# Kernel tuning notes

Hardware: AMD Instinct MI355X
Metric: run time of the kernel (lower is better)

Reference implementation:

```python
import jax, jax.numpy as jnp
import numpy as np

N_NODES = 50000
N_EDGES = 800000
HEADS = 6
LEAKY = 0.2


def gat_layer(x, W, a_src, a_dst, src, dst):
    """Multi-head GAT layer (Velickovic et al.), concat heads + ELU.
    x: [N, F_in], W: [H, F_in, F_out], a_src/a_dst: [H, F_out]."""
    n = x.shape[0]
    h = jnp.einsum('nf,hfo->nho', x, W)              # [N, H, F_out]
    es = jnp.einsum('nho,ho->nh', h, a_src)          # source attention term
    ed = jnp.einsum('nho,ho->nh', h, a_dst)          # destination attention term
    e = jax.nn.leaky_relu(es[src] + ed[dst], LEAKY)  # [E, H] per-edge logits
    # segment softmax over incoming edges of each destination node
    emax = jax.ops.segment_max(e, dst, num_segments=n)
    emax = jnp.where(jnp.isfinite(emax), emax, jnp.zeros_like(emax))
    ex = jnp.exp(e - emax[dst])                      # [E, H]
    denom = jax.ops.segment_sum(ex, dst, num_segments=n)
    alpha = ex / (denom[dst] + 1e-16)                # [E, H]
    msg = alpha[:, :, None] * h[src]                 # [E, H, F_out]
    out = jax.ops.segment_sum(msg, dst, num_segments=n)  # [N, H, F_out]
    return jax.nn.elu(out).reshape(n, -1)            # concat heads


def setup_inputs() -> dict:
    key = jax.random.key(0)
    ks = jax.random.split(key, 16)
    glorot = lambda k, shape: jax.random.normal(k, shape, jnp.float32) * np.sqrt(2.0 / (shape[-2] + shape[-1]))
    inp = {
        'x': jax.random.normal(ks[0], (N_NODES, 11), jnp.float32),
        'edge_index': jax.random.randint(ks[1], (2, N_EDGES), 0, N_NODES, jnp.int32),
        'W1': glorot(ks[2], (HEADS, 11, 16)),
        'a1s': glorot(ks[3], (HEADS, 16)),
        'a1d': glorot(ks[4], (HEADS, 16)),
        'W2': glorot(ks[5], (HEADS, 96, 32)),
        'a2s': glorot(ks[6], (HEADS, 32)),
        'a2d': glorot(ks[7], (HEADS, 32)),
        'W3': glorot(ks[8], (HEADS, 192, 64)),
        'a3s': glorot(ks[9], (HEADS, 64)),
        'a3d': glorot(ks[10], (HEADS, 64)),
        'Wd': glorot(ks[11], (384, 1)),
        'bd': jnp.zeros((1,), jnp.float32),
    }
    return inp


def reference(x, edge_index, W1, a1s, a1d, W2, a2s, a2d, W3, a3s, a3d, Wd, bd):
    src, dst = edge_index[0], edge_index[1]
    h = gat_layer(x, W1, a1s, a1d, src, dst)   # [N, 96]
    h = gat_layer(h, W2, a2s, a2d, src, dst)   # [N, 192]
    h = gat_layer(h, W3, a3s, a3d, src, dst)   # [N, 384]
    g = jnp.sum(h, axis=0).reshape(1, -1)      # sum pool -> [1, 384]
    g = g / jnp.maximum(jnp.linalg.norm(g, axis=1, keepdims=True), 1e-12)  # F.normalize
    out = g @ Wd + bd                          # Dense 384->1, linear nonlin
    return jnp.squeeze(out, 1)                 # [1]
```

## Files before the change

kernel.cpp:

```cpp
#include <hip/hip_runtime.h>
#include <hip/hip_bf16.h>


#define HHEADS 6

typedef __attribute__((ext_vector_type(8))) short bf16x8;
typedef __attribute__((ext_vector_type(4))) float f32x4;
typedef __attribute__((ext_vector_type(2))) float f32x2;

typedef __attribute__((address_space(3))) unsigned int lds_uint;
typedef const __attribute__((address_space(1))) unsigned int glb_uint;

__device__ __forceinline__ float bfl(unsigned u) { return __uint_as_float(u << 16); }
__device__ __forceinline__ float bfh(unsigned u) { return __uint_as_float(u & 0xffff0000u); }
__device__ __forceinline__ unsigned short f2bf(float v) {
    unsigned u = __float_as_uint(v);
    return (unsigned short)((u + 0x7fffu + ((u >> 16) & 1u)) >> 16);
}
__device__ __forceinline__ float bf2f(unsigned short h) {
    return __uint_as_float((unsigned)h << 16);
}
__device__ __forceinline__ unsigned fkey(float f) {
    unsigned u = __float_as_uint(f);
    return (u >> 31) ? ~u : (u | 0x80000000u);
}
__device__ __forceinline__ float funkey(unsigned k) {
    return (k >> 31) ? __uint_as_float(k & 0x7fffffffu) : __uint_as_float(~k);
}

__device__ __forceinline__ void xpose4(float& v0, float& v1, float& v2, float& v3, int b) {
    bool hi = (b & 2) != 0;
    float s0 = hi ? v0 : v2;
    float s1 = hi ? v1 : v3;
    s0 = __shfl_xor(s0, 2, 64);
    s1 = __shfl_xor(s1, 2, 64);
    v0 = hi ? s0 : v0;
    v1 = hi ? s1 : v1;
    v2 = hi ? v2 : s0;
    v3 = hi ? v3 : s1;
    bool od = (b & 1) != 0;
    float t0 = od ? v0 : v1;
    t0 = __shfl_xor(t0, 1, 64);
    v0 = od ? t0 : v0;
    v1 = od ? v1 : t0;
    float t1 = od ? v2 : v3;
    t1 = __shfl_xor(t1, 1, 64);
    v2 = od ? t1 : v2;
    v3 = od ? v3 : t1;
}

__global__ void zero_misc(int* __restrict__ count, int* __restrict__ cursor,
                          float* __restrict__ gmid, unsigned* __restrict__ gmax,
                          unsigned short* __restrict__ apH,
                          long pad3_off, long pad3_cnt, long pad6_off, long pad6_cnt, int n) {
    long i = (long)blockIdx.x * blockDim.x + threadIdx.x;
    long stride = (long)gridDim.x * blockDim.x;
    for (long j = i; j < n; j += stride) {
        count[j] = 0;
        cursor[j] = 0;
    }
    for (long j = i; j < 64 * 384; j += stride) gmid[j] = 0.f;
    if (i < 12) gmax[i] = 0u;
    for (long j = i; j < pad3_cnt; j += stride) apH[pad3_off + j] = 0;
    for (long j = i; j < pad6_cnt; j += stride) apH[pad6_off + j] = 0;
}

__global__ void hist_kernel(const int* __restrict__ dst, int* __restrict__ count, int E) {
    int e = blockIdx.x * blockDim.x + threadIdx.x;
    if (e >= E) return;
    atomicAdd(&count[dst[e]], 1);
}

__global__ void scan_block(const int* __restrict__ count, int* __restrict__ offsets,
                           int* __restrict__ bsum, int n) {
    __shared__ int s[1024];
    int i = blockIdx.x * 1024 + threadIdx.x;
    int v = (i < n) ? count[i] : 0;
    s[threadIdx.x] = v;
    __syncthreads();
    for (int off = 1; off < 1024; off <<= 1) {
        int t = (threadIdx.x >= (unsigned)off) ? s[threadIdx.x - off] : 0;
        __syncthreads();
        s[threadIdx.x] += t;
        __syncthreads();
    }
    if (i < n) offsets[i] = s[threadIdx.x] - v;
    if (threadIdx.x == 1023) bsum[blockIdx.x] = s[1023];
}

__global__ void scan_tops(int* __restrict__ bsum, int nb) {
    __shared__ int s[64];
    int t = threadIdx.x;
    int v = (t < nb) ? bsum[t] : 0;
    s[t] = v;
    __syncthreads();
    for (int off = 1; off < 64; off <<= 1) {
        int tmp = (t >= off) ? s[t - off] : 0;
        __syncthreads();
        s[t] += tmp;
        __syncthreads();
    }
    if (t < nb) bsum[t] = s[t] - v;
}

__global__ void scan_add(int* __restrict__ offsets, const int* __restrict__ bsum, int n,
                         int total) {
    int i = blockIdx.x * 1024 + threadIdx.x;
    if (i < n) offsets[i] += bsum[blockIdx.x];
    if (i == 0) offsets[n] = total;
}

__global__ void scatter_kernel(const int* __restrict__ src, const int* __restrict__ dst,
                               const int* __restrict__ offsets, int* __restrict__ cursor,
                               int* __restrict__ ssrc, int E) {
    int e = blockIdx.x * blockDim.x + threadIdx.x;
    if (e >= E) return;
    int d = dst[e];
    int pos = offsets[d] + atomicAdd(&cursor[d], 1);
    ssrc[pos] = src[e];
}

__global__ void repack_w(const float* __restrict__ W, float* __restrict__ Wp, int FIN, int F) {
    int HF = HHEADS * F;
    int i = blockIdx.x * blockDim.x + threadIdx.x;
    if (i >= FIN * HF) return;
    int k = i / HF, c = i % HF;
    int hd = c / F, f = c % F;
    Wp[i] = W[(hd * FIN + k) * F + f];
}

__global__ void repack_w_mfma(const float* __restrict__ W, unsigned short* __restrict__ bh,
                              int FIN, int F, int NPAD) {
    int i = blockIdx.x * blockDim.x + threadIdx.x;
    if (i >= FIN * NPAD) return;
    int k = i / NPAD, n = i % NPAD;
    int NKT = FIN / 32;
    int HF = HHEADS * F;
    float w = 0.f;
    if (n < HF) {
        int hd = n / F, f = n % F;
        w = W[(hd * FIN + k) * F + f];
    }
    size_t e = ((size_t)((n >> 4) * NKT + (k >> 5)) * 64 + ((n & 15) | (((k >> 3) & 3) << 4))) * 8 +
               (k & 7);
    bh[e] = f2bf(w);
}

template <int BM, int BN, int BK>
__global__ __launch_bounds__(256) void gemm_small_attn(const float* __restrict__ A,
                                                       const float* __restrict__ B,
                                                       unsigned char* __restrict__ C8,
                                                       const float* __restrict__ as_,
                                                       const float* __restrict__ ad_,
                                                       float* __restrict__ es,
                                                       float* __restrict__ ed, int M, int K,
                                                       int N) {
    __shared__ float As[BK][BM + 4];
    __shared__ float Bs[BK][BN];
    int tid = threadIdx.x;
    int tx = tid % 16, ty = tid / 16;
    int m0 = blockIdx.y * BM, n0 = blockIdx.x * BN;
    float acc[4][4] = {};
    for (int kk0 = 0; kk0 < K; kk0 += BK) {
#pragma unroll
        for (int i = 0; i < (BM * BK) / 256; ++i) {
            int idx = tid + i * 256;
            int m = idx / BK, k = idx % BK;
            float v = 0.f;
            if (m0 + m < M && kk0 + k < K) v = A[(size_t)(m0 + m) * K + kk0 + k];
            As[k][m] = v;
        }
#pragma unroll
        for (int i = 0; i < (BK * BN) / 1024; ++i) {
            int idx = tid + i * 256;
            int k = idx / (BN / 4), n4 = idx % (BN / 4);
            float4 v = make_float4(0.f, 0.f, 0.f, 0.f);
            if (kk0 + k < K && n0 + n4 * 4 < N)
                v = *(const float4*)&B[(size_t)(kk0 + k) * N + n0 + n4 * 4];
            *(float4*)&Bs[k][n4 * 4] = v;
        }
        __syncthreads();
#pragma unroll
        for (int k = 0; k < BK; ++k) {
            float4 av = *(const float4*)&As[k][ty * 4];
            float4 bv = *(const float4*)&Bs[k][tx * 4];
            float a[4] = {av.x, av.y, av.z, av.w};
            float b[4] = {bv.x, bv.y, bv.z, bv.w};
#pragma unroll
            for (int i = 0; i < 4; ++i)
#pragma unroll
                for (int j = 0; j < 4; ++j) acc[i][j] += a[i] * b[j];
        }
        __syncthreads();
    }
    bool colok = (n0 + tx * 4) < N;
    float asv[4], adv[4];
#pragma unroll
    for (int j = 0; j < 4; ++j) {
        int col = n0 + tx * 4 + j;
        asv[j] = (col < N) ? as_[col] : 0.f;
        adv[j] = (col < N) ? ad_[col] : 0.f;
    }
#pragma unroll
    for (int i = 0; i < 4; ++i) {
        int m = m0 + ty * 4 + i;
        bool mok = m < M;
        if (mok && colok) {
            int pk = __builtin_amdgcn_cvt_pk_fp8_f32(acc[i][0], acc[i][1], 0, false);
            pk = __builtin_amdgcn_cvt_pk_fp8_f32(acc[i][2], acc[i][3], pk, true);
            *(unsigned*)&C8[(size_t)m * N + n0 + tx * 4] = (unsigned)pk;
        }
        float ps = 0.f, pd = 0.f;
#pragma unroll
        for (int j = 0; j < 4; ++j) {
            ps += acc[i][j] * asv[j];
            pd += acc[i][j] * adv[j];
        }
        ps += __shfl_down(ps, 2, 4);
        ps += __shfl_down(ps, 1, 4);
        pd += __shfl_down(pd, 2, 4);
        pd += __shfl_down(pd, 1, 4);
        if (mok && colok && (tx & 3) == 0) {
            int hd = (n0 + tx * 4) >> 4;
            es[(size_t)m * HHEADS + hd] = ps;
            ed[(size_t)m * HHEADS + hd] = pd;
        }
    }
}

template <int K, int NREAL, int NPAD, int F, int MT>
__global__ __launch_bounds__(256) void gemm_attn_mfma(
    const unsigned short* __restrict__ Ah, const unsigned short* __restrict__ Bh,
    unsigned char* __restrict__ C8, const float* __restrict__ as_,
    const float* __restrict__ ad_, float* __restrict__ es, float* __restrict__ ed,
    unsigned* __restrict__ gmax, int M) {
    constexpr int NKT = K / 32;
    __shared__ unsigned short sB[NKT * 4096];
    __shared__ unsigned short sA[2][4096];
    int tid = threadIdx.x;
    int lane = tid & 63, wave = tid >> 6;
    int wrow = wave >> 1, wcol = wave & 1;
    int quad = lane >> 4, c16 = lane & 15;

    int nwg = gridDim.x * gridDim.y;
    int hh = blockIdx.y * gridDim.x + blockIdx.x;
    int q = nwg >> 3, r = nwg & 7;
    int xcd = hh & 7, pos = hh >> 3;
    int wk = (xcd < r ? xcd * (q + 1) : r * (q + 1) + (xcd - r) * q) + pos;
    int bx = wk % gridDim.x, by = wk / gridDim.x;

    int n0 = bx * 128;
    int bn16 = n0 >> 4;
    int nmt = (M + 127) >> 7;

#pragma unroll
    for (int kt2 = 0; kt2 < NKT; ++kt2) {
#pragma unroll
        for (int rep = 0; rep < 2; ++rep) {
            int chunk = tid + rep * 256;
            int tile = chunk >> 6, e8 = chunk & 63;
            size_t boff = ((size_t)((bn16 + tile) * NKT + kt2) * 64 + e8) * 8;
            __builtin_amdgcn_global_load_lds((glb_uint*)&Bh[boff],
                                             (lds_uint*)&sB[kt2 * 4096 + chunk * 8], 16, 0, 0);
        }
    }
    auto STAGE_A = [&](int mti, int kt2, int buf) {
#pragma unroll
        for (int rep = 0; rep < 2; ++rep) {
            int chunk = tid + rep * 256;
            int tile = chunk >> 6, e8 = chunk & 63;
            size_t aoff = ((size_t)((mti * 8 + tile) * NKT + kt2) * 64 + e8) * 8;
            __builtin_amdgcn_global_load_lds((glb_uint*)&Ah[aoff],
                                             (lds_uint*)&sA[buf][chunk * 8], 16, 0, 0);
        }
    };
    STAGE_A(min(by * MT, nmt - 1), 0, 0);
    asm volatile("s_waitcnt vmcnt(0)" ::: "memory");
    __builtin_amdgcn_s_barrier();

    float asv[4], adv[4];
#pragma unroll
    for (int j = 0; j < 4; ++j) {
        int col = n0 + wcol * 64 + j * 16 + c16;
        bool ok = col < NREAL;
        asv[j] = ok ? as_[col] : 0.f;
        adv[j] = ok ? ad_[col] : 0.f;
    }
    float mx = -1e30f;
    float mxA = -1e30f, mxB = -1e30f;
    bool colvalid = (n0 + wcol * 64) < NREAL;
    int b4 = lane & 3;

    f32x4 acc[4][4] = {};
    const int T = MT * NKT;
    int mt = 0, kt = 0;
    for (int t = 0; t < T; ++t) {
        int cur = t & 1;
        int nkt = kt + 1, nmt2 = mt;
        if (nkt == NKT) {
            nkt = 0;
            nmt2 = mt + 1;
        }
        if (t + 1 < T) STAGE_A(min(by * MT + nmt2, nmt - 1), nkt, cur ^ 1);
        bf16x8 fah[4], fbh[4];
#pragma unroll
        for (int i = 0; i < 4; ++i) {
            fah[i] = *(const bf16x8*)&sA[cur][(wrow * 4 + i) * 512 + lane * 8];
            fbh[i] = *(const bf16x8*)&sB[kt * 4096 + (wcol * 4 + i) * 512 + lane * 8];
        }
        asm volatile("s_waitcnt lgkmcnt(0)" ::: "memory");
        __builtin_amdgcn_sched_barrier(0);
#pragma unroll
        for (int i = 0; i < 4; ++i)
#pragma unroll
            for (int j = 0; j < 4; ++j)
                acc[i][j] = __builtin_amdgcn_mfma_f32_16x16x32_bf16(fah[i], fbh[j], acc[i][j],
                                                                    0, 0, 0);
        if (kt == NKT - 1) {
            int m0 = (by * MT + mt) * 128;
            if (m0 < M) {
#pragma unroll
                for (int i = 0; i < 4; ++i) {
#pragma unroll
                    for (int r2 = 0; r2 < 4; ++r2) {
                        int m = m0 + wrow * 64 + i * 16 + quad * 4 + r2;
                        bool mok = m < M;
                        if (F == 64) {
                            float ps = acc[i][0][r2] * asv[0] + acc[i][1][r2] * asv[1] +
                                       acc[i][2][r2] * asv[2] + acc[i][3][r2] * asv[3];
                            float pd = acc[i][0][r2] * adv[0] + acc[i][1][r2] * adv[1] +
                                       acc[i][2][r2] * adv[2] + acc[i][3][r2] * adv[3];
#pragma unroll
                            for (int off = 8; off > 0; off >>= 1) {
                                ps += __shfl_down(ps, off, 16);
                                pd += __shfl_down(pd, off, 16);
                            }
                            if (mok && c16 == 0) {
                                int hd = (n0 + wcol * 64) / 64;
                                es[(size_t)m * HHEADS + hd] = ps;
                                ed[(size_t)m * HHEADS + hd] = pd;
                                mx = fmaxf(mx, ps);
                            }
                        } else {
                            float psA = acc[i][0][r2] * asv[0] + acc[i][1][r2] * asv[1];
                            float pdA = acc[i][0][r2] * adv[0] + acc[i][1][r2] * adv[1];
                            float psB = acc[i][2][r2] * asv[2] + acc[i][3][r2] * asv[3];
                            float pdB = acc[i][2][r2] * adv[2] + acc[i][3][r2] * adv[3];
#pragma unroll
                            for (int off = 8; off > 0; off >>= 1) {
                                psA += __shfl_down(psA, off, 16);
                                pdA += __shfl_down(pdA, off, 16);
                                psB += __shfl_down(psB, off, 16);
                                pdB += __shfl_down(pdB, off, 16);
                            }
                            if (mok && c16 == 0 && colvalid) {
                                int colbase = n0 + wcol * 64;
                                int hd = colbase / 32;
                                es[(size_t)m * HHEADS + hd] = psA;
                                ed[(size_t)m * HHEADS + hd] = pdA;
                                es[(size_t)m * HHEADS + hd + 1] = psB;
                                ed[(size_t)m * HHEADS + hd + 1] = pdB;
                                mxA = fmaxf(mxA, psA);
                                mxB = fmaxf(mxB, psB);
                            }
                        }
                    }
                }
#pragma unroll
                for (int i = 0; i < 4; ++i) {
                    int m = m0 + wrow * 64 + i * 16 + quad * 4 + b4;
                    bool mok = m < M;
#pragma unroll
                    for (int j = 0; j < 4; ++j) {
                        float v0 = acc[i][j][0], v1 = acc[i][j][1], v2 = acc[i][j][2],
                              v3 = acc[i][j][3];
                        xpose4(v0, v1, v2, v3, b4);
                        int colb = n0 + wcol * 64 + j * 16 + (c16 & 12);
                        if (mok && (F == 64 || colvalid)) {
                            int pk = __builtin_amdgcn_cvt_pk_fp8_f32(v0, v1, 0, false);
                            pk = __builtin_amdgcn_cvt_pk_fp8_f32(v2, v3, pk, true);
                            *(unsigned*)&C8[(size_t)m * NREAL + colb] = (unsigned)pk;
                        }
                    }
                }
            }
#pragma unroll
            for (int i = 0; i < 4; ++i)
#pragma unroll
                for (int j = 0; j < 4; ++j) acc[i][j] = (f32x4){0.f, 0.f, 0.f, 0.f};
        }
        asm volatile("s_waitcnt vmcnt(0)" ::: "memory");
        __builtin_amdgcn_s_barrier();
        kt = nkt;
        mt = nmt2;
    }

    if (F == 64) {
#pragma unroll
        for (int off = 32; off > 0; off >>= 1) mx = fmaxf(mx, __shfl_xor(mx, off));
        if (lane == 0) atomicMax(&gmax[(n0 + wcol * 64) / 64], fkey(mx));
    } else {
        mxA = fmaxf(mxA, __shfl_xor(mxA, 16));
        mxA = fmaxf(mxA, __shfl_xor(mxA, 32));
        mxB = fmaxf(mxB, __shfl_xor(mxB, 16));
        mxB = fmaxf(mxB, __shfl_xor(mxB, 32));
        if (lane == 0 && colvalid) {
            int hd = (n0 + wcol * 64) / 32;
            atomicMax(&gmax[6 + hd], fkey(mxA));
            atomicMax(&gmax[6 + hd + 1], fkey(mxB));
        }
    }
}

template <int F>
__global__ __launch_bounds__(256) void aggregate_fused(
    const unsigned char* __restrict__ h8, const float* __restrict__ es,
    const float* __restrict__ ed, const int* __restrict__ offsets,
    const int* __restrict__ ssrc, unsigned short* __restrict__ oh, int n) {
    constexpr int HF = HHEADS * F;
    constexpr int C8 = HF / 8;
    int tid = blockIdx.x * blockDim.x + threadIdx.x;
    if (tid >= n * C8) return;
    int node = tid / C8, q = tid % C8;
    int c = q * 8, hd = c / F;
    int a = offsets[node], b = offsets[node + 1];
    float edv = ed[node * HHEADS + hd];
    float m = -1e30f, l = 0.f;
    f32x2 a0 = {0.f, 0.f}, a1 = {0.f, 0.f}, a2 = {0.f, 0.f}, a3 = {0.f, 0.f};
    for (int j = a; j < b; ++j) {
        int s = ssrc[j];
        float v = es[s * HHEADS + hd] + edv;
        v = v > 0.f ? v : 0.2f * v;
        float mn = fmaxf(m, v);
        float r = __expf(m - mn);
        float wgt = __expf(v - mn);
        uint2 hv = *(const uint2*)&h8[(size_t)s * HF + c];
        f32x2 p0 = __builtin_amdgcn_cvt_pk_f32_fp8((int)hv.x, false);
        f32x2 p1 = __builtin_amdgcn_cvt_pk_f32_fp8((int)hv.x, true);
        f32x2 p2 = __builtin_amdgcn_cvt_pk_f32_fp8((int)hv.y, false);
        f32x2 p3 = __builtin_amdgcn_cvt_pk_f32_fp8((int)hv.y, true);
        l = l * r + wgt;
        f32x2 rv = {r, r}, wv = {wgt, wgt};
        a0 = a0 * rv + wv * p0;
        a1 = a1 * rv + wv * p1;
        a2 = a2 * rv + wv * p2;
        a3 = a3 * rv + wv * p3;
        m = mn;
    }
    float invd = 1.0f / (l + 1e-16f);
    float res[8] = {a0[0], a0[1], a1[0], a1[1], a2[0], a2[1], a3[0], a3[1]};
    unsigned short th[8];
#pragma unroll
    for (int k = 0; k < 8; ++k) {
        float v = res[k] * invd;
        v = v > 0.f ? v : (__expf(v) - 1.0f);
        th[k] = f2bf(v);
    }
    constexpr int NKT = HF / 32;
    int lq = (node & 15) | (((c >> 3) & 3) << 4);
    size_t base = ((size_t)((node >> 4) * NKT + (c >> 5)) * 64 + lq) * 8;
    *(uint4*)&oh[base] = *(uint4*)th;
}

__global__ __launch_bounds__(256) void aggregate_wpn2(
    const unsigned char* __restrict__ h8, const float* __restrict__ es,
    const float* __restrict__ ed, const unsigned* __restrict__ gmax,
    const int* __restrict__ offsets, const int* __restrict__ ssrc,
    unsigned short* __restrict__ oh, int n) {
    constexpr int HF = 192;
    int wid = (int)((blockIdx.x * (unsigned)blockDim.x + threadIdx.x) >> 6);
    int lane = threadIdx.x & 63;
    if (wid >= n || lane >= 48) return;
    int node = wid;
    int hd = lane >> 3;
    int c = lane * 4;
    int a = offsets[node], b = offsets[node + 1];
    float edv = ed[node * HHEADS + hd];
    float mv = funkey(gmax[6 + hd]) + edv;
    float m = mv > 0.f ? mv : 0.2f * mv;
    float l = 0.f;
    f32x2 a0 = {0.f, 0.f}, a1 = {0.f, 0.f};
    const unsigned char* hbase = h8 + c;
    int j = a;
    for (; j + 3 < b; j += 4) {
        int s0 = ssrc[j], s1 = ssrc[j + 1], s2 = ssrc[j + 2], s3 = ssrc[j + 3];
        float ev0 = es[(size_t)s0 * HHEADS + hd];
        float ev1 = es[(size_t)s1 * HHEADS + hd];
        float ev2 = es[(size_t)s2 * HHEADS + hd];
        float ev3 = es[(size_t)s3 * HHEADS + hd];
        unsigned h0 = *(const unsigned*)(hbase + (size_t)s0 * HF);
        unsigned h1 = *(const unsigned*)(hbase + (size_t)s1 * HF);
        unsigned h2 = *(const unsigned*)(hbase + (size_t)s2 * HF);
        unsigned h3 = *(const unsigned*)(hbase + (size_t)s3 * HF);
        float v0 = ev0 + edv;
        v0 = v0 > 0.f ? v0 : 0.2f * v0;
        float v1 = ev1 + edv;
        v1 = v1 > 0.f ? v1 : 0.2f * v1;
        float v2 = ev2 + edv;
        v2 = v2 > 0.f ? v2 : 0.2f * v2;
        float v3 = ev3 + edv;
        v3 = v3 > 0.f ? v3 : 0.2f * v3;
        float w0 = __expf(v0 - m);
        float w1 = __expf(v1 - m);
        float w2 = __expf(v2 - m);
        float w3 = __expf(v3 - m);
        {
            f32x2 p0 = __builtin_amdgcn_cvt_pk_f32_fp8((int)h0, false);
            f32x2 p1 = __builtin_amdgcn_cvt_pk_f32_fp8((int)h0, true);
            f32x2 wv = {w0, w0};
            l += w0;
            a0 = a0 + wv * p0;
            a1 = a1 + wv * p1;
        }
        {
            f32x2 p0 = __builtin_amdgcn_cvt_pk_f32_fp8((int)h1, false);
            f32x2 p1 = __builtin_amdgcn_cvt_pk_f32_fp8((int)h1, true);
            f32x2 wv = {w1, w1};
            l += w1;
            a0 = a0 + wv * p0;
            a1 = a1 + wv * p1;
        }
        {
            f32x2 p0 = __builtin_amdgcn_cvt_pk_f32_fp8((int)h2, false);
            f32x2 p1 = __builtin_amdgcn_cvt_pk_f32_fp8((int)h2, true);
            f32x2 wv = {w2, w2};
            l += w2;
            a0 = a0 + wv * p0;
            a1 = a1 + wv * p1;
        }
        {
            f32x2 p0 = __builtin_amdgcn_cvt_pk_f32_fp8((int)h3, false);
            f32x2 p1 = __builtin_amdgcn_cvt_pk_f32_fp8((int)h3, true);
            f32x2 wv = {w3, w3};
            l += w3;
            a0 = a0 + wv * p0;
            a1 = a1 + wv * p1;
        }
    }
    for (; j < b; ++j) {
        int s0 = ssrc[j];
        float ev0 = es[(size_t)s0 * HHEADS + hd];
        unsigned h0 = *(const unsigned*)(hbase + (size_t)s0 * HF);
        float v0 = ev0 + edv;
        v0 = v0 > 0.f ? v0 : 0.2f * v0;
        float w0 = __expf(v0 - m);
        f32x2 p0 = __builtin_amdgcn_cvt_pk_f32_fp8((int)h0, false);
        f32x2 p1 = __builtin_amdgcn_cvt_pk_f32_fp8((int)h0, true);
        f32x2 wv = {w0, w0};
        l += w0;
        a0 = a0 + wv * p0;
        a1 = a1 + wv * p1;
    }
    float invd = 1.0f / (l + 1e-16f);
    float res[4] = {a0[0], a0[1], a1[0], a1[1]};
    unsigned short th[4];
#pragma unroll
    for (int k = 0; k < 4; ++k) {
        float v = res[k] * invd;
        v = v > 0.f ? v : (__expf(v) - 1.0f);
        th[k] = f2bf(v);
    }
    int lq = (node & 15) | (((c >> 3) & 3) << 4);
    size_t base = ((size_t)((node >> 4) * (HF / 32) + (c >> 5)) * 64 + lq) * 8 + (c & 7);
    *(uint2*)&oh[base] = *(uint2*)th;
}

__global__ __launch_bounds__(256) void aggregate_wpn3(
    const unsigned char* __restrict__ h8, const float* __restrict__ es,
    const float* __restrict__ ed, const unsigned* __restrict__ gmax,
    const int* __restrict__ offsets, const int* __restrict__ ssrc,
    float* __restrict__ gmid, int n) {
    constexpr int HF = 384;
    __shared__ float gp[4][384];
    int wave = threadIdx.x >> 6, lane = threadIdx.x & 63;
    int wid = blockIdx.x * 4 + wave;
    int node = wid;
    int hd = lane >> 3;
    int c = lane * 8;
    bool active = (wid < n) && (lane < 48);
    float res[8] = {};
    if (active) {
        int a = offsets[node], b = offsets[node + 1];
        float edv = ed[node * HHEADS + hd];
        float mv = funkey(gmax[hd]) + edv;
        float m = mv > 0.f ? mv : 0.2f * mv;
        float l = 0.f;
        f32x2 a0 = {0.f, 0.f}, a1 = {0.f, 0.f}, a2 = {0.f, 0.f}, a3 = {0.f, 0.f};
        const unsigned char* hbase = h8 + c;
        int j = a;
        for (; j + 3 < b; j += 4) {
            int s0 = ssrc[j], s1 = ssrc[j + 1], s2 = ssrc[j + 2], s3 = ssrc[j + 3];
            float ev0 = es[(size_t)s0 * HHEADS + hd];
            float ev1 = es[(size_t)s1 * HHEADS + hd];
            float ev2 = es[(size_t)s2 * HHEADS + hd];
            float ev3 = es[(size_t)s3 * HHEADS + hd];
            uint2 h0 = *(const uint2*)(hbase + (size_t)s0 * HF);
            uint2 h1 = *(const uint2*)(hbase + (size_t)s1 * HF);
            uint2 h2 = *(const uint2*)(hbase + (size_t)s2 * HF);
            uint2 h3 = *(const uint2*)(hbase + (size_t)s3 * HF);
            float v0 = ev0 + edv;
            v0 = v0 > 0.f ? v0 : 0.2f * v0;
            float v1 = ev1 + edv;
            v1 = v1 > 0.f ? v1 : 0.2f * v1;
            float v2 = ev2 + edv;
            v2 = v2 > 0.f ? v2 : 0.2f * v2;
            float v3 = ev3 + edv;
            v3 = v3 > 0.f ? v3 : 0.2f * v3;
            float w0 = __expf(v0 - m);
            float w1 = __expf(v1 - m);
            float w2 = __expf(v2 - m);
            float w3 = __expf(v3 - m);
            {
                f32x2 p0 = __builtin_amdgcn_cvt_pk_f32_fp8((int)h0.x, false);
                f32x2 p1 = __builtin_amdgcn_cvt_pk_f32_fp8((int)h0.x, true);
                f32x2 p2 = __builtin_amdgcn_cvt_pk_f32_fp8((int)h0.y, false);
                f32x2 p3 = __builtin_amdgcn_cvt_pk_f32_fp8((int)h0.y, true);
                f32x2 wv = {w0, w0};
                l += w0;
                a0 = a0 + wv * p0;
                a1 = a1 + wv * p1;
                a2 = a2 + wv * p2;
                a3 = a3 + wv * p3;
            }
            {
                f32x2 p0 = __builtin_amdgcn_cvt_pk_f32_fp8((int)h1.x, false);
                f32x2 p1 = __builtin_amdgcn_cvt_pk_f32_fp8((int)h1.x, true);
                f32x2 p2 = __builtin_amdgcn_cvt_pk_f32_fp8((int)h1.y, false);
                f32x2 p3 = __builtin_amdgcn_cvt_pk_f32_fp8((int)h1.y, true);
                f32x2 wv = {w1, w1};
                l += w1;
                a0 = a0 + wv * p0;
                a1 = a1 + wv * p1;
                a2 = a2 + wv * p2;
                a3 = a3 + wv * p3;
            }
            {
                f32x2 p0 = __builtin_amdgcn_cvt_pk_f32_fp8((int)h2.x, false);
                f32x2 p1 = __builtin_amdgcn_cvt_pk_f32_fp8((int)h2.x, true);
                f32x2 p2 = __builtin_amdgcn_cvt_pk_f32_fp8((int)h2.y, false);
                f32x2 p3 = __builtin_amdgcn_cvt_pk_f32_fp8((int)h2.y, true);
                f32x2 wv = {w2, w2};
                l += w2;
                a0 = a0 + wv * p0;
                a1 = a1 + wv * p1;
                a2 = a2 + wv * p2;
                a3 = a3 + wv * p3;
            }
            {
                f32x2 p0 = __builtin_amdgcn_cvt_pk_f32_fp8((int)h3.x, false);
                f32x2 p1 = __builtin_amdgcn_cvt_pk_f32_fp8((int)h3.x, true);
                f32x2 p2 = __builtin_amdgcn_cvt_pk_f32_fp8((int)h3.y, false);
                f32x2 p3 = __builtin_amdgcn_cvt_pk_f32_fp8((int)h3.y, true);
                f32x2 wv = {w3, w3};
                l += w3;
                a0 = a0 + wv * p0;
                a1 = a1 + wv * p1;
                a2 = a2 + wv * p2;
                a3 = a3 + wv * p3;
            }
        }
        for (; j < b; ++j) {
            int s0 = ssrc[j];
            float ev0 = es[(size_t)s0 * HHEADS + hd];
            uint2 h0 = *(const uint2*)(hbase + (size_t)s0 * HF);
            float v0 = ev0 + edv;
            v0 = v0 > 0.f ? v0 : 0.2f * v0;
            float w0 = __expf(v0 - m);
            f32x2 p0 = __builtin_amdgcn_cvt_pk_f32_fp8((int)h0.x, false);
            f32x2 p1 = __builtin_amdgcn_cvt_pk_f32_fp8((int)h0.x, true);
            f32x2 p2 = __builtin_amdgcn_cvt_pk_f32_fp8((int)h0.y, false);
            f32x2 p3 = __builtin_amdgcn_cvt_pk_f32_fp8((int)h0.y, true);
            f32x2 wv = {w0, w0};
            l += w0;
            a0 = a0 + wv * p0;
            a1 = a1 + wv * p1;
            a2 = a2 + wv * p2;
            a3 = a3 + wv * p3;
        }
        float invd = 1.0f / (l + 1e-16f);
        float t[8] = {a0[0], a0[1], a1[0], a1[1], a2[0], a2[1], a3[0], a3[1]};
#pragma unroll
        for (int k = 0; k < 8; ++k) {
            float v = t[k] * invd;
            res[k] = v > 0.f ? v : (__expf(v) - 1.0f);
        }
    }
    if (lane < 48) {
#pragma unroll
        for (int k = 0; k < 8; ++k) gp[wave][c + k] = res[k];
    }
    __syncthreads();
    int rep = blockIdx.x & 63;
    for (int i = threadIdx.x; i < 384; i += 256) {
        float s = gp[0][i] + gp[1][i] + gp[2][i] + gp[3][i];
        atomicAdd(&gmid[rep * 384 + i], s);
    }
}

__global__ void final_kernel(const float* __restrict__ gmid, const float* __restrict__ Wd,
                             const float* __restrict__ bd, float* __restrict__ outp) {
    __shared__ float red[384];
    int t = threadIdx.x;
    float v = 0.f;
    for (int r = 0; r < 64; ++r) v += gmid[r * 384 + t];
    red[t] = v * v;
    __syncthreads();
    for (int s = 192; s >= 3; s >>= 1) {
        if (t < s) red[t] += red[t + s];
        __syncthreads();
    }
    __shared__ float scale_s;
    if (t == 0) {
        float norm = sqrtf(red[0] + red[1] + red[2]);
        scale_s = 1.0f / fmaxf(norm, 1e-12f);
    }
    __syncthreads();
    float scale = scale_s;
    red[t] = v * scale * Wd[t];
    __syncthreads();
    for (int s = 192; s >= 3; s >>= 1) {
        if (t < s) red[t] += red[t + s];
        __syncthreads();
    }
    if (t == 0) outp[0] = red[0] + red[1] + red[2] + bd[0];
}

extern "C" void kernel_launch(void* const* d_in, const int* in_sizes, int n_in, void* d_out,
                              int out_size, void* d_ws, size_t ws_size, hipStream_t stream) {
    const float* x = (const float*)d_in[0];
    const int* ei = (const int*)d_in[1];
    const float* W1 = (const float*)d_in[2];
    const float* a1s = (const float*)d_in[3];
    const float* a1d = (const float*)d_in[4];
    const float* W2 = (const float*)d_in[5];
    const float* a2s = (const float*)d_in[6];
    const float* a2d = (const float*)d_in[7];
    const float* W3 = (const float*)d_in[8];
    const float* a3s = (const float*)d_in[9];
    const float* a3d = (const float*)d_in[10];
    const float* Wd = (const float*)d_in[11];
    const float* bd = (const float*)d_in[12];
    float* outp = (float*)d_out;

    const int N = in_sizes[0] / 11;
    const int E = in_sizes[1] / 2;
    const int* src = ei;
    const int* dst = ei + E;

    const int NT16 = ((N + 127) / 128) * 8;
    const int NMT = (N + 127) / 128;

    char* w = (char*)d_ws;
    size_t off = 0;
    auto A = [&](size_t bytes) {
        size_t o = off;
        off += (bytes + 255) & ~(size_t)255;
        return o;
    };
    unsigned char* bufH = (unsigned char*)(w + A((size_t)N * 384 * 2));
    float* gmid = (float*)(w + A((size_t)N * 384 * 2));
    unsigned short* apH = (unsigned short*)(w + A((size_t)NT16 * 6 * 512 * 2));
    unsigned short* b2H = (unsigned short*)(w + A((size_t)16 * 3 * 512 * 2));
    unsigned short* b3H = (unsigned short*)(w + A((size_t)24 * 6 * 512 * 2));
    float* es = (float*)(w + A((size_t)N * HHEADS * 4));
    float* ed = (float*)(w + A((size_t)N * HHEADS * 4));
    unsigned* gmax = (unsigned*)(w + A(256));
    float* wp = (float*)(w + A((size_t)11 * 96 * 4));
    int* count = (int*)(w + A((size_t)(N + 1) * 4));
    int* cursor = (int*)(w + A((size_t)(N + 1) * 4));
    int* offsets = (int*)(w + A((size_t)(N + 1) * 4));
    int* bsum = (int*)(w + A(64 * 4));
    int* ssrc = (int*)(w + A((size_t)E * 4));

    const long t16v = N / 16;
    const long padT = NT16 - t16v;
    zero_misc<<<(N + 255) / 256, 256, 0, stream>>>(count, cursor, gmid, gmax, apH,
                                                   t16v * 3 * 512, padT * 3 * 512,
                                                   t16v * 6 * 512, padT * 6 * 512, N);

    hist_kernel<<<(E + 255) / 256, 256, 0, stream>>>(dst, count, E);
    int nb = (N + 1023) / 1024;
    scan_block<<<nb, 1024, 0, stream>>>(count, offsets, bsum, N);
    scan_tops<<<1, 64, 0, stream>>>(bsum, nb);
    scan_add<<<nb, 1024, 0, stream>>>(offsets, bsum, N, E);
    scatter_kernel<<<(E + 255) / 256, 256, 0, stream>>>(src, dst, offsets, cursor, ssrc, E);

    repack_w<<<(11 * 96 + 255) / 256, 256, 0, stream>>>(W1, wp, 11, 16);
    repack_w_mfma<<<(96 * 256 + 255) / 256, 256, 0, stream>>>(W2, b2H, 96, 32, 256);
    repack_w_mfma<<<(192 * 384 + 255) / 256, 256, 0, stream>>>(W3, b3H, 192, 64, 384);

    {
        dim3 grid((96 + 63) / 64, (N + 63) / 64);
        gemm_small_attn<64, 64, 32><<<grid, 256, 0, stream>>>(x, wp, bufH, a1s, a1d, es, ed, N,
                                                              11, 96);
    }
    {
        long total = (long)N * (96 / 8);
        aggregate_fused<16><<<(total + 255) / 256, 256, 0, stream>>>(bufH, es, ed, offsets,
                                                                     ssrc, apH, N);
    }

    {
        dim3 grid(2, (NMT + 3) / 4);
        gemm_attn_mfma<96, 192, 256, 32, 4><<<grid, 256, 0, stream>>>(apH, b2H, bufH, a2s,
                                                                      a2d, es, ed, gmax, N);
    }
    {
        int grid = (N + 3) / 4;
        aggregate_wpn2<<<grid, 256, 0, stream>>>(bufH, es, ed, gmax, offsets, ssrc, apH, N);
    }

    {
        dim3 grid(3, (NMT + 3) / 4);
        gemm_attn_mfma<192, 384, 384, 64, 4><<<grid, 256, 0, stream>>>(apH, b3H, bufH, a3s,
                                                                       a3d, es, ed, gmax, N);
    }
    {
        int grid = (N + 3) / 4;
        aggregate_wpn3<<<grid, 256, 0, stream>>>(bufH, es, ed, gmax, offsets, ssrc, gmid, N);
    }

    final_kernel<<<1, 384, 0, stream>>>(gmid, Wd, bd, outp);
}
```

Baseline: 432.5 us.

## Replace LDS-staged MFMA GEMM with per-wave direct-from-global tiles

The layer-2 and layer-3 feature GEMMs no longer stage A and B through LDS with double buffering and barriers. Each wave now computes an independent 64x64 output tile, loading its MFMA fragments straight from global memory, and the attention-score and fp8 epilogue is kept but runs per wave. This removes LDS traffic, barriers and the serial multi-tile loop, and launches many more small workgroups for parallelism. In exchange, B tiles are re-read from global or L2 by every wave, there is no prefetch overlap, and there are more atomicMax operations on gmax.

```diff
diff --git a/kernel.cpp b/kernel.cpp
--- a/kernel.cpp
+++ b/kernel.cpp
@@ -7,9 +7,6 @@
 typedef __attribute__((ext_vector_type(8))) short bf16x8;
 typedef __attribute__((ext_vector_type(4))) float f32x4;
 typedef __attribute__((ext_vector_type(2))) float f32x2;
-
-typedef __attribute__((address_space(3))) unsigned int lds_uint;
-typedef const __attribute__((address_space(1))) unsigned int glb_uint;
 
 __device__ __forceinline__ float bfl(unsigned u) { return __uint_as_float(u << 16); }
 __device__ __forceinline__ float bfh(unsigned u) { return __uint_as_float(u & 0xffff0000u); }
@@ -228,186 +225,124 @@
     }
 }
 
-template <int K, int NREAL, int NPAD, int F, int MT>
-__global__ __launch_bounds__(256) void gemm_attn_mfma(
+template <int K, int NREAL, int F>
+__global__ __launch_bounds__(256) void gemm_attn_dw(
     const unsigned short* __restrict__ Ah, const unsigned short* __restrict__ Bh,
     unsigned char* __restrict__ C8, const float* __restrict__ as_,
     const float* __restrict__ ad_, float* __restrict__ es, float* __restrict__ ed,
-    unsigned* __restrict__ gmax, int M) {
+    unsigned* __restrict__ gmax, int M, int nwaves, int nstrips) {
     constexpr int NKT = K / 32;
-    __shared__ unsigned short sB[NKT * 4096];
-    __shared__ unsigned short sA[2][4096];
-    int tid = threadIdx.x;
-    int lane = tid & 63, wave = tid >> 6;
-    int wrow = wave >> 1, wcol = wave & 1;
-    int quad = lane >> 4, c16 = lane & 15;
-
-    int nwg = gridDim.x * gridDim.y;
-    int hh = blockIdx.y * gridDim.x + blockIdx.x;
-    int q = nwg >> 3, r = nwg & 7;
-    int xcd = hh & 7, pos = hh >> 3;
-    int wk = (xcd < r ? xcd * (q + 1) : r * (q + 1) + (xcd - r) * q) + pos;
-    int bx = wk % gridDim.x, by = wk / gridDim.x;
-
-    int n0 = bx * 128;
-    int bn16 = n0 >> 4;
-    int nmt = (M + 127) >> 7;
-
-#pragma unroll
-    for (int kt2 = 0; kt2 < NKT; ++kt2) {
-#pragma unroll
-        for (int rep = 0; rep < 2; ++rep) {
-            int chunk = tid + rep * 256;
-            int tile = chunk >> 6, e8 = chunk & 63;
-            size_t boff = ((size_t)((bn16 + tile) * NKT + kt2) * 64 + e8) * 8;
-            __builtin_amdgcn_global_load_lds((glb_uint*)&Bh[boff],
-                                             (lds_uint*)&sB[kt2 * 4096 + chunk * 8], 16, 0, 0);
-        }
-    }
-    auto STAGE_A = [&](int mti, int kt2, int buf) {
-#pragma unroll
-        for (int rep = 0; rep < 2; ++rep) {
-            int chunk = tid + rep * 256;
-            int tile = chunk >> 6, e8 = chunk & 63;
-            size_t aoff = ((size_t)((mti * 8 + tile) * NKT + kt2) * 64 + e8) * 8;
-            __builtin_amdgcn_global_load_lds((glb_uint*)&Ah[aoff],
-                                             (lds_uint*)&sA[buf][chunk * 8], 16, 0, 0);
-        }
-    };
-    STAGE_A(min(by * MT, nmt - 1), 0, 0);
-    asm volatile("s_waitcnt vmcnt(0)" ::: "memory");
-    __builtin_amdgcn_s_barrier();
+    int gw = blockIdx.x * 4 + (threadIdx.x >> 6);
+    if (gw >= nwaves) return;
+    int lane = threadIdx.x & 63;
+    int quad = lane >> 4, c16 = lane & 15, b4 = lane & 3;
+    int strip = gw / nstrips, cs = gw - strip * nstrips;
+    int n0 = cs * 64;
+    int at16 = strip * 4, bt16 = cs * 4;
+
+    f32x4 acc[4][4] = {};
+#pragma unroll
+    for (int kt = 0; kt < NKT; ++kt) {
+        bf16x8 fah[4], fbh[4];
+#pragma unroll
+        for (int i = 0; i < 4; ++i)
+            fah[i] = *(const bf16x8*)&Ah[((size_t)(at16 + i) * NKT + kt) * 512 + lane * 8];
+#pragma unroll
+        for (int j = 0; j < 4; ++j)
+            fbh[j] = *(const bf16x8*)&Bh[((size_t)(bt16 + j) * NKT + kt) * 512 + lane * 8];
+#pragma unroll
+        for (int i = 0; i < 4; ++i)
+#pragma unroll
+            for (int j = 0; j < 4; ++j)
+                acc[i][j] = __builtin_amdgcn_mfma_f32_16x16x32_bf16(fah[i], fbh[j], acc[i][j],
+                                                                    0, 0, 0);
+    }
 
     float asv[4], adv[4];
 #pragma unroll
     for (int j = 0; j < 4; ++j) {
-        int col = n0 + wcol * 64 + j * 16 + c16;
+        int col = n0 + j * 16 + c16;
         bool ok = col < NREAL;
         asv[j] = ok ? as_[col] : 0.f;
         adv[j] = ok ? ad_[col] : 0.f;
     }
     float mx = -1e30f;
     float mxA = -1e30f, mxB = -1e30f;
-    bool colvalid = (n0 + wcol * 64) < NREAL;
-    int b4 = lane & 3;
-
-    f32x4 acc[4][4] = {};
-    const int T = MT * NKT;
-    int mt = 0, kt = 0;
-    for (int t = 0; t < T; ++t) {
-        int cur = t & 1;
-        int nkt = kt + 1, nmt2 = mt;
-        if (nkt == NKT) {
-            nkt = 0;
-            nmt2 = mt + 1;
-        }
-        if (t + 1 < T) STAGE_A(min(by * MT + nmt2, nmt - 1), nkt, cur ^ 1);
-        bf16x8 fah[4], fbh[4];
-#pragma unroll
-        for (int i = 0; i < 4; ++i) {
-            fah[i] = *(const bf16x8*)&sA[cur][(wrow * 4 + i) * 512 + lane * 8];
-            fbh[i] = *(const bf16x8*)&sB[kt * 4096 + (wcol * 4 + i) * 512 + lane * 8];
-        }
-        asm volatile("s_waitcnt lgkmcnt(0)" ::: "memory");
-        __builtin_amdgcn_sched_barrier(0);
-#pragma unroll
-        for (int i = 0; i < 4; ++i)
-#pragma unroll
-            for (int j = 0; j < 4; ++j)
-                acc[i][j] = __builtin_amdgcn_mfma_f32_16x16x32_bf16(fah[i], fbh[j], acc[i][j],
-                                                                    0, 0, 0);
-        if (kt == NKT - 1) {
-            int m0 = (by * MT + mt) * 128;
-            if (m0 < M) {
-#pragma unroll
-                for (int i = 0; i < 4; ++i) {
-#pragma unroll
-                    for (int r2 = 0; r2 < 4; ++r2) {
-                        int m = m0 + wrow * 64 + i * 16 + quad * 4 + r2;
-                        bool mok = m < M;
-                        if (F == 64) {
-                            float ps = acc[i][0][r2] * asv[0] + acc[i][1][r2] * asv[1] +
-                                       acc[i][2][r2] * asv[2] + acc[i][3][r2] * asv[3];
-                            float pd = acc[i][0][r2] * adv[0] + acc[i][1][r2] * adv[1] +
-                                       acc[i][2][r2] * adv[2] + acc[i][3][r2] * adv[3];
-#pragma unroll
-                            for (int off = 8; off > 0; off >>= 1) {
-                                ps += __shfl_down(ps, off, 16);
-                                pd += __shfl_down(pd, off, 16);
-                            }
-                            if (mok && c16 == 0) {
-                                int hd = (n0 + wcol * 64) / 64;
-                                es[(size_t)m * HHEADS + hd] = ps;
-                                ed[(size_t)m * HHEADS + hd] = pd;
-                                mx = fmaxf(mx, ps);
-                            }
-                        } else {
-                            float psA = acc[i][0][r2] * asv[0] + acc[i][1][r2] * asv[1];
-                            float pdA = acc[i][0][r2] * adv[0] + acc[i][1][r2] * adv[1];
-                            float psB = acc[i][2][r2] * asv[2] + acc[i][3][r2] * asv[3];
-                            float pdB = acc[i][2][r2] * adv[2] + acc[i][3][r2] * adv[3];
-#pragma unroll
-                            for (int off = 8; off > 0; off >>= 1) {
-                                psA += __shfl_down(psA, off, 16);
-                                pdA += __shfl_down(pdA, off, 16);
-                                psB += __shfl_down(psB, off, 16);
-                                pdB += __shfl_down(pdB, off, 16);
-                            }
-                            if (mok && c16 == 0 && colvalid) {
-                                int colbase = n0 + wcol * 64;
-                                int hd = colbase / 32;
-                                es[(size_t)m * HHEADS + hd] = psA;
-                                ed[(size_t)m * HHEADS + hd] = pdA;
-                                es[(size_t)m * HHEADS + hd + 1] = psB;
-                                ed[(size_t)m * HHEADS + hd + 1] = pdB;
-                                mxA = fmaxf(mxA, psA);
-                                mxB = fmaxf(mxB, psB);
-                            }
-                        }
-                    }
+
+#pragma unroll
+    for (int i = 0; i < 4; ++i) {
+#pragma unroll
+        for (int r2 = 0; r2 < 4; ++r2) {
+            int m = strip * 64 + i * 16 + quad * 4 + r2;
+            bool mok = m < M;
+            if (F == 64) {
+                float ps = acc[i][0][r2] * asv[0] + acc[i][1][r2] * asv[1] +
+                           acc[i][2][r2] * asv[2] + acc[i][3][r2] * asv[3];
+                float pd = acc[i][0][r2] * adv[0] + acc[i][1][r2] * adv[1] +
+                           acc[i][2][r2] * adv[2] + acc[i][3][r2] * adv[3];
+#pragma unroll
+                for (int off = 8; off > 0; off >>= 1) {
+                    ps += __shfl_down(ps, off, 16);
+                    pd += __shfl_down(pd, off, 16);
                 }
-#pragma unroll
-                for (int i = 0; i < 4; ++i) {
-                    int m = m0 + wrow * 64 + i * 16 + quad * 4 + b4;
-                    bool mok = m < M;
-#pragma unroll
-                    for (int j = 0; j < 4; ++j) {
-                        float v0 = acc[i][j][0], v1 = acc[i][j][1], v2 = acc[i][j][2],
-                              v3 = acc[i][j][3];
-                        xpose4(v0, v1, v2, v3, b4);
-                        int colb = n0 + wcol * 64 + j * 16 + (c16 & 12);
-                        if (mok && (F == 64 || colvalid)) {
-                            int pk = __builtin_amdgcn_cvt_pk_fp8_f32(v0, v1, 0, false);
-                            pk = __builtin_amdgcn_cvt_pk_fp8_f32(v2, v3, pk, true);
-                            *(unsigned*)&C8[(size_t)m * NREAL + colb] = (unsigned)pk;
-                        }
-                    }
+                if (mok && c16 == 0) {
+                    es[(size_t)m * HHEADS + cs] = ps;
+                    ed[(size_t)m * HHEADS + cs] = pd;
+                    mx = fmaxf(mx, ps);
+                }
+            } else {
+                float psA = acc[i][0][r2] * asv[0] + acc[i][1][r2] * asv[1];
+                float pdA = acc[i][0][r2] * adv[0] + acc[i][1][r2] * adv[1];
+                float psB = acc[i][2][r2] * asv[2] + acc[i][3][r2] * asv[3];
+                float pdB = acc[i][2][r2] * adv[2] + acc[i][3][r2] * adv[3];
+#pragma unroll
+                for (int off = 8; off > 0; off >>= 1) {
+                    psA += __shfl_down(psA, off, 16);
+                    pdA += __shfl_down(pdA, off, 16);
+                    psB += __shfl_down(psB, off, 16);
+                    pdB += __shfl_down(pdB, off, 16);
+                }
+                if (mok && c16 == 0) {
+                    int hd = cs * 2;
+                    es[(size_t)m * HHEADS + hd] = psA;
+                    ed[(size_t)m * HHEADS + hd] = pdA;
+                    es[(size_t)m * HHEADS + hd + 1] = psB;
+                    ed[(size_t)m * HHEADS + hd + 1] = pdB;
+                    mxA = fmaxf(mxA, psA);
+                    mxB = fmaxf(mxB, psB);
                 }
             }
-#pragma unroll
-            for (int i = 0; i < 4; ++i)
-#pragma unroll
-                for (int j = 0; j < 4; ++j) acc[i][j] = (f32x4){0.f, 0.f, 0.f, 0.f};
-        }
-        asm volatile("s_waitcnt vmcnt(0)" ::: "memory");
-        __builtin_amdgcn_s_barrier();
-        kt = nkt;
-        mt = nmt2;
-    }
-
+        }
+    }
     if (F == 64) {
 #pragma unroll
         for (int off = 32; off > 0; off >>= 1) mx = fmaxf(mx, __shfl_xor(mx, off));
-        if (lane == 0) atomicMax(&gmax[(n0 + wcol * 64) / 64], fkey(mx));
+        if (lane == 0) atomicMax(&gmax[cs], fkey(mx));
     } else {
         mxA = fmaxf(mxA, __shfl_xor(mxA, 16));
         mxA = fmaxf(mxA, __shfl_xor(mxA, 32));
         mxB = fmaxf(mxB, __shfl_xor(mxB, 16));
         mxB = fmaxf(mxB, __shfl_xor(mxB, 32));
-        if (lane == 0 && colvalid) {
-            int hd = (n0 + wcol * 64) / 32;
-            atomicMax(&gmax[6 + hd], fkey(mxA));
-            atomicMax(&gmax[6 + hd + 1], fkey(mxB));
+        if (lane == 0) {
+            atomicMax(&gmax[6 + cs * 2], fkey(mxA));
+            atomicMax(&gmax[6 + cs * 2 + 1], fkey(mxB));
+        }
+    }
+
+#pragma unroll
+    for (int i = 0; i < 4; ++i) {
+        int m = strip * 64 + i * 16 + quad * 4 + b4;
+        bool mok = m < M;
+#pragma unroll
+        for (int j = 0; j < 4; ++j) {
+            float v0 = acc[i][j][0], v1 = acc[i][j][1], v2 = acc[i][j][2], v3 = acc[i][j][3];
+            xpose4(v0, v1, v2, v3, b4);
+            int colb = n0 + j * 16 + (c16 & 12);
+            if (mok) {
+                int pk = __builtin_amdgcn_cvt_pk_fp8_f32(v0, v1, 0, false);
+                pk = __builtin_amdgcn_cvt_pk_fp8_f32(v2, v3, pk, true);
+                *(unsigned*)&C8[(size_t)m * NREAL + colb] = (unsigned)pk;
+            }
         }
     }
 }
@@ -748,7 +683,7 @@
     const int* dst = ei + E;
 
     const int NT16 = ((N + 127) / 128) * 8;
-    const int NMT = (N + 127) / 128;
+    const int NM64 = (N + 63) / 64;
 
     char* w = (char*)d_ws;
     size_t off = 0;
@@ -801,9 +736,9 @@
     }
 
     {
-        dim3 grid(2, (NMT + 3) / 4);
-        gemm_attn_mfma<96, 192, 256, 32, 4><<<grid, 256, 0, stream>>>(apH, b2H, bufH, a2s,
-                                                                      a2d, es, ed, gmax, N);
+        int nw = NM64 * 3;
+        gemm_attn_dw<96, 192, 32><<<(nw + 3) / 4, 256, 0, stream>>>(apH, b2H, bufH, a2s, a2d,
+                                                                    es, ed, gmax, N, nw, 3);
     }
     {
         int grid = (N + 3) / 4;
@@ -811,9 +746,9 @@
     }
 
     {
-        dim3 grid(3, (NMT + 3) / 4);
-        gemm_attn_mfma<192, 384, 384, 64, 4><<<grid, 256, 0, stream>>>(apH, b3H, bufH, a3s,
-                                                                       a3d, es, ed, gmax, N);
+        int nw = NM64 * 6;
+        gemm_attn_dw<192, 384, 64><<<(nw + 3) / 4, 256, 0, stream>>>(apH, b3H, bufH, a3s, a3d,
+                                                                     es, ed, gmax, N, nw, 6);
     }
     {
         int grid = (N + 3) / 4;
```

Measured after the change: 462.1 us. 6.9% more time.

## Double-buffer whole M-tile A panels instead of per-K-slice staging in GAT GEMM

Applied to the files above, without the earlier changes.

The GEMM+attention kernel now stages the entire K extent of each 128-row A tile into LDS at once and double-buffers across M tiles, instead of double-buffering per 32-wide K slice. The inner K loop becomes fully unrolled with no barriers or vmcnt waits between K steps, so there is one sync per M tile rather than one per K step. The cost is roughly NKT times more LDS for sA, which may reduce occupancy for the larger-K layers. The explicit lgkmcnt wait and sched_barrier are dropped, leaving instruction scheduling to the compiler.

```diff
diff --git a/kernel.cpp b/kernel.cpp
--- a/kernel.cpp
+++ b/kernel.cpp
@@ -236,7 +236,7 @@
     unsigned* __restrict__ gmax, int M) {
     constexpr int NKT = K / 32;
     __shared__ unsigned short sB[NKT * 4096];
-    __shared__ unsigned short sA[2][4096];
+    __shared__ unsigned short sA[2][NKT * 4096];
     int tid = threadIdx.x;
     int lane = tid & 63, wave = tid >> 6;
     int wrow = wave >> 1, wcol = wave & 1;
@@ -264,19 +264,22 @@
                                              (lds_uint*)&sB[kt2 * 4096 + chunk * 8], 16, 0, 0);
         }
     }
-    auto STAGE_A = [&](int mti, int kt2, int buf) {
-#pragma unroll
-        for (int rep = 0; rep < 2; ++rep) {
-            int chunk = tid + rep * 256;
-            int tile = chunk >> 6, e8 = chunk & 63;
-            size_t aoff = ((size_t)((mti * 8 + tile) * NKT + kt2) * 64 + e8) * 8;
-            __builtin_amdgcn_global_load_lds((glb_uint*)&Ah[aoff],
-                                             (lds_uint*)&sA[buf][chunk * 8], 16, 0, 0);
+    auto STAGE_AMT = [&](int mti, int buf) {
+#pragma unroll
+        for (int kt2 = 0; kt2 < NKT; ++kt2) {
+#pragma unroll
+            for (int rep = 0; rep < 2; ++rep) {
+                int chunk = tid + rep * 256;
+                int tile = chunk >> 6, e8 = chunk & 63;
+                size_t aoff = ((size_t)((mti * 8 + tile) * NKT + kt2) * 64 + e8) * 8;
+                __builtin_amdgcn_global_load_lds(
+                    (glb_uint*)&Ah[aoff], (lds_uint*)&sA[buf][kt2 * 4096 + chunk * 8], 16, 0,
+                    0);
+            }
         }
     };
-    STAGE_A(min(by * MT, nmt - 1), 0, 0);
-    asm volatile("s_waitcnt vmcnt(0)" ::: "memory");
-    __builtin_amdgcn_s_barrier();
+    STAGE_AMT(min(by * MT, nmt - 1), 0);
+    __syncthreads();
 
     float asv[4], adv[4];
 #pragma unroll
@@ -291,32 +294,27 @@
     bool colvalid = (n0 + wcol * 64) < NREAL;
     int b4 = lane & 3;
 
-    f32x4 acc[4][4] = {};
-    const int T = MT * NKT;
-    int mt = 0, kt = 0;
-    for (int t = 0; t < T; ++t) {
-        int cur = t & 1;
-        int nkt = kt + 1, nmt2 = mt;
-        if (nkt == NKT) {
-            nkt = 0;
-            nmt2 = mt + 1;
-        }
-        if (t + 1 < T) STAGE_A(min(by * MT + nmt2, nmt - 1), nkt, cur ^ 1);
-        bf16x8 fah[4], fbh[4];
-#pragma unroll
-        for (int i = 0; i < 4; ++i) {
-            fah[i] = *(const bf16x8*)&sA[cur][(wrow * 4 + i) * 512 + lane * 8];
-            fbh[i] = *(const bf16x8*)&sB[kt * 4096 + (wcol * 4 + i) * 512 + lane * 8];
-        }
-        asm volatile("s_waitcnt lgkmcnt(0)" ::: "memory");
-        __builtin_amdgcn_sched_barrier(0);
-#pragma unroll
-        for (int i = 0; i < 4; ++i)
-#pragma unroll
-            for (int j = 0; j < 4; ++j)
-                acc[i][j] = __builtin_amdgcn_mfma_f32_16x16x32_bf16(fah[i], fbh[j], acc[i][j],
-                                                                    0, 0, 0);
-        if (kt == NKT - 1) {
+    for (int mt = 0; mt < MT; ++mt) {
+        int cur = mt & 1;
+        if (mt + 1 < MT) STAGE_AMT(min(by * MT + mt + 1, nmt - 1), cur ^ 1);
+        const unsigned short* sAc = sA[cur];
+        f32x4 acc[4][4] = {};
+#pragma unroll
+        for (int kt = 0; kt < NKT; ++kt) {
+            bf16x8 fah[4], fbh[4];
+#pragma unroll
+            for (int i = 0; i < 4; ++i) {
+                fah[i] = *(const bf16x8*)&sAc[kt * 4096 + (wrow * 4 + i) * 512 + lane * 8];
+                fbh[i] = *(const bf16x8*)&sB[kt * 4096 + (wcol * 4 + i) * 512 + lane * 8];
+            }
+#pragma unroll
+            for (int i = 0; i < 4; ++i)
+#pragma unroll
+                for (int j = 0; j < 4; ++j)
+                    acc[i][j] = __builtin_amdgcn_mfma_f32_16x16x32_bf16(fah[i], fbh[j],
+                                                                        acc[i][j], 0, 0, 0);
+        }
+        {
             int m0 = (by * MT + mt) * 128;
             if (m0 < M) {
 #pragma unroll
@@ -384,15 +382,8 @@
                     }
                 }
             }
-#pragma unroll
-            for (int i = 0; i < 4; ++i)
-#pragma unroll
-                for (int j = 0; j < 4; ++j) acc[i][j] = (f32x4){0.f, 0.f, 0.f, 0.f};
-        }
-        asm volatile("s_waitcnt vmcnt(0)" ::: "memory");
-        __builtin_amdgcn_s_barrier();
-        kt = nkt;
-        mt = nmt2;
+        }
+        __syncthreads();
     }
 
     if (F == 64) {
```

New measurement: 434.5 us. No clear change (+0.5%).
